# Kernel optimization log

Hardware: AMD Instinct MI355X
Metric: run time of the kernel (lower is better)

The kernel has to match this reference:

```python
import jax, jax.numpy as jnp
import numpy as np

EPS = 1e-5

def layer_norm(x, gamma, beta):
    mu = jnp.mean(x, axis=-1, keepdims=True)
    var = jnp.mean(jnp.square(x - mu), axis=-1, keepdims=True)
    return (x - mu) * jax.lax.rsqrt(var + EPS) * gamma + beta

def reverse_sigmoid(x):
    # torch version clamps value to [0.001, 0.999] with a detached offset ->
    # straight-through: clipped value, identity gradient into the logit.
    y = x + jax.lax.stop_gradient(jnp.clip(x, 0.001, 0.999) - x)
    return jnp.log(y) - jnp.log1p(-y)

def setup_inputs() -> dict:
    key = jax.random.key(0)
    ks = jax.random.split(key, 8)
    N, D, A, F8, FD = 32768, 1024, 256, 8, 64
    inp = {
        "unary_term": jax.random.normal(ks[0], (N, D), jnp.float32),
        "pair_term": jax.random.normal(ks[1], (N, D), jnp.float32),
        "auxiliary_term": jax.random.normal(ks[2], (N, A), jnp.float32),
        "auxiliary_gating_weight": jax.random.uniform(ks[3], (N,), jnp.float32),
        # self.w params: LayerNorm(2D) + Linear(2D, FD)
        "ln_gamma": jnp.ones((2 * D,), jnp.float32),
        "ln_beta": jnp.zeros((2 * D,), jnp.float32),
        "W": jax.random.normal(ks[4], (2 * D, FD), jnp.float32) * 0.02,
        "b": jnp.zeros((FD,), jnp.float32),
        # self.w_aux params: LayerNorm(A) + Linear(A, 8)
        "ln_aux_gamma": jnp.ones((A,), jnp.float32),
        "ln_aux_beta": jnp.zeros((A,), jnp.float32),
        "W_aux": jax.random.normal(ks[5], (A, F8), jnp.float32) * 0.02,
        "b_aux": jnp.zeros((F8,), jnp.float32),
        # use_auxiliary_gate_weight=True -> both init to 0.33
        "gate_weight": jnp.array(0.33, jnp.float32),
        "aux_gate_weight": jnp.array(0.33, jnp.float32),
    }
    return inp

def reference(unary_term, pair_term, auxiliary_term, auxiliary_gating_weight,
              ln_gamma, ln_beta, W, b, ln_aux_gamma, ln_aux_beta, W_aux, b_aux,
              gate_weight, aux_gate_weight):
    # paired_feats = relu(cat([unary, pair], 1))
    paired = jax.nn.relu(jnp.concatenate([unary_term, pair_term], axis=1))  # [N, 2D]
    # gate = sigmoid(Linear(relu(LN(paired))))
    gate = jax.nn.sigmoid(jax.nn.relu(layer_norm(paired, ln_gamma, ln_beta)) @ W + b)  # [N, FD]
    aux_gate = jax.nn.sigmoid(jax.nn.relu(layer_norm(auxiliary_term, ln_aux_gamma, ln_aux_beta)) @ W_aux + b_aux)  # [N, 8]
    gate = jnp.mean(gate, axis=1)        # [N]
    aux_gate = jnp.mean(aux_gate, axis=1)  # [N]
    logit = gate_weight * reverse_sigmoid(gate) + aux_gate_weight * reverse_sigmoid(aux_gate)
    g = jax.nn.sigmoid(logit) * auxiliary_gating_weight  # use_auxiliary_gate_weight=True
    output = pair_term * g[:, None]
    return (output, g)
```

## Files before the change

### kernel.cpp

```cpp
#include <hip/hip_runtime.h>
#include <math.h>


#define EPS_LN 1e-5f

typedef __attribute__((ext_vector_type(8))) short short8;
typedef __attribute__((ext_vector_type(4))) float f32x4;

__device__ __forceinline__ unsigned short f2bf(float f) {
  unsigned int u = __float_as_uint(f);
  u += 0x7FFFu + ((u >> 16) & 1u);
  return (unsigned short)(u >> 16);
}

__device__ __forceinline__ float wsum64(float v) {
  v += __shfl_xor(v, 32);
  v += __shfl_xor(v, 16);
  v += __shfl_xor(v, 8);
  v += __shfl_xor(v, 4);
  v += __shfl_xor(v, 2);
  v += __shfl_xor(v, 1);
  return v;
}

__device__ __forceinline__ float sigmoidf_(float x) {
  return 1.0f / (1.0f + __expf(-x));
}

__device__ __forceinline__ float rsigf(float x) {
  float y = fminf(fmaxf(x, 0.001f), 0.999f);
  return logf(y) - log1pf(-y);
}

__device__ __forceinline__ ushort4 norm_pack(float4 x, float4 g, float4 b,
                                             float mu, float rstd) {
  ushort4 o;
  o.x = f2bf(fmaxf((x.x - mu) * rstd * g.x + b.x, 0.f));
  o.y = f2bf(fmaxf((x.y - mu) * rstd * g.y + b.y, 0.f));
  o.z = f2bf(fmaxf((x.z - mu) * rstd * g.z + b.z, 0.f));
  o.w = f2bf(fmaxf((x.w - mu) * rstd * g.w + b.w, 0.f));
  return o;
}

__global__ void prep_wfrag(const float* __restrict__ W,
                           unsigned short* __restrict__ wfrag) {
  const int lane = threadIdx.x;
  const int b = blockIdx.x;
  const int ntile = b >> 6;
  const int kb = b & 63;
  const int f = (ntile << 4) + (lane & 15);
  const int kbase = (kb << 5) + ((lane >> 4) << 3);
  unsigned short tmp[8];
#pragma unroll
  for (int j = 0; j < 8; ++j) tmp[j] = f2bf(W[(size_t)(kbase + j) * 64 + f]);
  ushort4* dst = reinterpret_cast<ushort4*>(wfrag + (((size_t)b * 64 + lane) << 3));
  dst[0] = make_ushort4(tmp[0], tmp[1], tmp[2], tmp[3]);
  dst[1] = make_ushort4(tmp[4], tmp[5], tmp[6], tmp[7]);
}

__global__ void __launch_bounds__(256, 2) fused_main(
    const float* __restrict__ unary, const float* __restrict__ pair,
    const float* __restrict__ aux, const float* __restrict__ auxw,
    const float* __restrict__ ln_g, const float* __restrict__ ln_b,
    const float* __restrict__ b_lin,
    const float* __restrict__ ln_ag, const float* __restrict__ ln_ab,
    const float* __restrict__ W_aux, const float* __restrict__ b_aux,
    const float* __restrict__ gw, const float* __restrict__ agw,
    const unsigned short* __restrict__ wfrag,
    float* __restrict__ out, float* __restrict__ out_g) {
  __shared__ unsigned short act_lds[16 * 2048];

  const int tid = threadIdx.x;
  const int w = tid >> 6;
  const int lane = tid & 63;
  const int base = blockIdx.x << 4;

  float auxg0 = 0.f, auxg1 = 0.f, auxg2 = 0.f, auxg3 = 0.f;

#pragma unroll
  for (int i = 0; i < 4; ++i) {
    const int rl = (w << 2) + i;
    const int row = base + rl;
    const int sw = rl & 7;

    const float4* u4 = reinterpret_cast<const float4*>(unary + (size_t)row * 1024);
    const float4* p4 = reinterpret_cast<const float4*>(pair + (size_t)row * 1024);
    float4 uv[4], pv[4];
#pragma unroll
    for (int j = 0; j < 4; ++j) {
      uv[j] = u4[lane + 64 * j];
      pv[j] = p4[lane + 64 * j];
    }
    float s = 0.f, sq = 0.f;
#pragma unroll
    for (int j = 0; j < 4; ++j) {
      uv[j].x = fmaxf(uv[j].x, 0.f); uv[j].y = fmaxf(uv[j].y, 0.f);
      uv[j].z = fmaxf(uv[j].z, 0.f); uv[j].w = fmaxf(uv[j].w, 0.f);
      pv[j].x = fmaxf(pv[j].x, 0.f); pv[j].y = fmaxf(pv[j].y, 0.f);
      pv[j].z = fmaxf(pv[j].z, 0.f); pv[j].w = fmaxf(pv[j].w, 0.f);
      s += uv[j].x + uv[j].y + uv[j].z + uv[j].w;
      s += pv[j].x + pv[j].y + pv[j].z + pv[j].w;
      sq += uv[j].x * uv[j].x + uv[j].y * uv[j].y + uv[j].z * uv[j].z + uv[j].w * uv[j].w;
      sq += pv[j].x * pv[j].x + pv[j].y * pv[j].y + pv[j].z * pv[j].z + pv[j].w * pv[j].w;
    }
    s = wsum64(s);
    sq = wsum64(sq);
    const float mu = s * (1.f / 2048.f);
    const float rstd = rsqrtf(sq * (1.f / 2048.f) - mu * mu + EPS_LN);

    const float4* g4 = reinterpret_cast<const float4*>(ln_g);
    const float4* bb4 = reinterpret_cast<const float4*>(ln_b);
#pragma unroll
    for (int j = 0; j < 4; ++j) {
      const int idx = lane + 64 * j;
      const int off = (lane & 1) << 2;
      ushort4 o = norm_pack(uv[j], g4[idx], bb4[idx], mu, rstd);
      int addr = (rl << 11) + ((((idx >> 1)) ^ sw) << 3) + off;
      *reinterpret_cast<ushort4*>(&act_lds[addr]) = o;
      ushort4 o2 = norm_pack(pv[j], g4[256 + idx], bb4[256 + idx], mu, rstd);
      int addr2 = (rl << 11) + (((128 + (idx >> 1)) ^ sw) << 3) + off;
      *reinterpret_cast<ushort4*>(&act_lds[addr2]) = o2;
    }

    const float4 av = reinterpret_cast<const float4*>(aux + (size_t)row * 256)[lane];
    float as = av.x + av.y + av.z + av.w;
    float asq = av.x * av.x + av.y * av.y + av.z * av.z + av.w * av.w;
    as = wsum64(as);
    asq = wsum64(asq);
    const float amu = as * (1.f / 256.f);
    const float arstd = rsqrtf(asq * (1.f / 256.f) - amu * amu + EPS_LN);
    const float4 ag = reinterpret_cast<const float4*>(ln_ag)[lane];
    const float4 ab = reinterpret_cast<const float4*>(ln_ab)[lane];
    float aa[4];
    aa[0] = fmaxf((av.x - amu) * arstd * ag.x + ab.x, 0.f);
    aa[1] = fmaxf((av.y - amu) * arstd * ag.y + ab.y, 0.f);
    aa[2] = fmaxf((av.z - amu) * arstd * ag.z + ab.z, 0.f);
    aa[3] = fmaxf((av.w - amu) * arstd * ag.w + ab.w, 0.f);
    float pf[8];
#pragma unroll
    for (int f = 0; f < 8; ++f) pf[f] = 0.f;
#pragma unroll
    for (int t = 0; t < 4; ++t) {
      const float4* wr = reinterpret_cast<const float4*>(W_aux + (((size_t)lane << 2) + t) * 8);
      float4 wa = wr[0], wb = wr[1];
      pf[0] += aa[t] * wa.x; pf[1] += aa[t] * wa.y;
      pf[2] += aa[t] * wa.z; pf[3] += aa[t] * wa.w;
      pf[4] += aa[t] * wb.x; pf[5] += aa[t] * wb.y;
      pf[6] += aa[t] * wb.z; pf[7] += aa[t] * wb.w;
    }
    float ss = 0.f;
#pragma unroll
    for (int f = 0; f < 8; ++f) {
      float v = wsum64(pf[f]);
      ss += sigmoidf_(v + b_aux[f]);
    }
    const float agv = ss * (1.f / 8.f);
    if (i == 0) auxg0 = agv;
    else if (i == 1) auxg1 = agv;
    else if (i == 2) auxg2 = agv;
    else auxg3 = agv;
  }

  __syncthreads();

  f32x4 acc = {0.f, 0.f, 0.f, 0.f};
  const int arow = lane & 15;
  const int quad = lane >> 4;
  const int abase = arow << 11;
  const int asw = arow & 7;
  const unsigned short* wbase = wfrag + ((size_t)(w << 6) << 9);
#pragma unroll 8
  for (int kb = 0; kb < 64; ++kb) {
    const int c = (kb << 2) + quad;
    const short8 afrag =
        *reinterpret_cast<const short8*>(&act_lds[abase + ((c ^ asw) << 3)]);
    const short8 bfrag =
        *reinterpret_cast<const short8*>(wbase + ((size_t)kb << 9) + (lane << 3));
    acc = __builtin_amdgcn_mfma_f32_16x16x32_bf16(afrag, bfrag, acc, 0, 0, 0);
  }

  const float bl = b_lin[(w << 4) + arow];
  float sred[4];
#pragma unroll
  for (int i = 0; i < 4; ++i) {
    float v = sigmoidf_(acc[i] + bl);
    v += __shfl_xor(v, 1);
    v += __shfl_xor(v, 2);
    v += __shfl_xor(v, 4);
    v += __shfl_xor(v, 8);
    sred[i] = v;
  }

  __syncthreads();
  float* gate_part = reinterpret_cast<float*>(act_lds);
  if (arow == 0) {
#pragma unroll
    for (int i = 0; i < 4; ++i)
      gate_part[(w << 4) + (quad << 2) + i] = sred[i];
  }
  __syncthreads();

  const float gwt = gw[0];
  const float agwt = agw[0];
#pragma unroll
  for (int i = 0; i < 4; ++i) {
    const int rl = (w << 2) + i;
    const int row = base + rl;
    const float gsum = gate_part[rl] + gate_part[16 + rl] +
                       gate_part[32 + rl] + gate_part[48 + rl];
    const float gate = gsum * (1.f / 64.f);
    const float auxg = (i == 0) ? auxg0 : (i == 1) ? auxg1 : (i == 2) ? auxg2 : auxg3;
    const float logit = gwt * rsigf(gate) + agwt * rsigf(auxg);
    const float g = sigmoidf_(logit) * auxw[row];

    const float4* p4 = reinterpret_cast<const float4*>(pair + (size_t)row * 1024);
    float4* o4 = reinterpret_cast<float4*>(out + (size_t)row * 1024);
#pragma unroll
    for (int j = 0; j < 4; ++j) {
      float4 pv = p4[lane + 64 * j];
      pv.x *= g; pv.y *= g; pv.z *= g; pv.w *= g;
      o4[lane + 64 * j] = pv;
    }
    if (lane == 0) out_g[row] = g;
  }
}

extern "C" void kernel_launch(void* const* d_in, const int* in_sizes, int n_in,
                              void* d_out, int out_size, void* d_ws, size_t ws_size,
                              hipStream_t stream) {
  const float* unary = (const float*)d_in[0];
  const float* pair  = (const float*)d_in[1];
  const float* aux   = (const float*)d_in[2];
  const float* auxw  = (const float*)d_in[3];
  const float* ln_g  = (const float*)d_in[4];
  const float* ln_b  = (const float*)d_in[5];
  const float* W     = (const float*)d_in[6];
  const float* b     = (const float*)d_in[7];
  const float* ln_ag = (const float*)d_in[8];
  const float* ln_ab = (const float*)d_in[9];
  const float* W_aux = (const float*)d_in[10];
  const float* b_aux = (const float*)d_in[11];
  const float* gw    = (const float*)d_in[12];
  const float* agw   = (const float*)d_in[13];

  const int N = in_sizes[3];
  unsigned short* wfrag = (unsigned short*)d_ws;
  float* out = (float*)d_out;
  float* out_g = out + (size_t)N * 1024;

  prep_wfrag<<<256, 64, 0, stream>>>(W, wfrag);
  fused_main<<<N / 16, 256, 0, stream>>>(unary, pair, aux, auxw, ln_g, ln_b, b,
                                         ln_ag, ln_ab, W_aux, b_aux, gw, agw,
                                         wfrag, out, out_g);
}
```

Before: 480.0 us.

## Drop activation LDS staging; recompute normalized inputs straight into MFMA fragments

The 64KB bf16 activation buffer in shared memory is replaced by small per-row stats and a partial-sum array. In the GEMM phase each wave re-reads its quarter of the K dimension from global memory (expected L2 hits), normalizes it in registers, and feeds four N-tiles of MFMA, with cross-wave K partials reduced through LDS. The smaller LDS footprint allows the launch bound to rise to 4 blocks per CU. The aux-gate reduction is also restructured to use fewer shuffles. The cost is a second read of unary/pair rows and extra normalization arithmetic.

Result: faster. 435.8 us (-9.2%).

```diff
diff --git a/kernel.cpp b/kernel.cpp
--- a/kernel.cpp
+++ b/kernel.cpp
@@ -32,14 +32,12 @@
   return logf(y) - log1pf(-y);
 }
 
-__device__ __forceinline__ ushort4 norm_pack(float4 x, float4 g, float4 b,
-                                             float mu, float rstd) {
-  ushort4 o;
-  o.x = f2bf(fmaxf((x.x - mu) * rstd * g.x + b.x, 0.f));
-  o.y = f2bf(fmaxf((x.y - mu) * rstd * g.y + b.y, 0.f));
-  o.z = f2bf(fmaxf((x.z - mu) * rstd * g.z + b.z, 0.f));
-  o.w = f2bf(fmaxf((x.w - mu) * rstd * g.w + b.w, 0.f));
-  return o;
+__device__ __forceinline__ short nrm1(float x, float g, float b,
+                                      float rs, float nmr) {
+  float t = fmaxf(x, 0.f);
+  float n = fmaf(t, rs, nmr);
+  float z = fmaxf(fmaf(n, g, b), 0.f);
+  return (short)f2bf(z);
 }
 
 __global__ void prep_wfrag(const float* __restrict__ W,
@@ -58,7 +56,7 @@
   dst[1] = make_ushort4(tmp[4], tmp[5], tmp[6], tmp[7]);
 }
 
-__global__ void __launch_bounds__(256, 2) fused_main(
+__global__ void __launch_bounds__(256, 4) fused_main(
     const float* __restrict__ unary, const float* __restrict__ pair,
     const float* __restrict__ aux, const float* __restrict__ auxw,
     const float* __restrict__ ln_g, const float* __restrict__ ln_b,
@@ -68,7 +66,9 @@
     const float* __restrict__ gw, const float* __restrict__ agw,
     const unsigned short* __restrict__ wfrag,
     float* __restrict__ out, float* __restrict__ out_g) {
-  __shared__ unsigned short act_lds[16 * 2048];
+  __shared__ float part[4][16][68];
+  __shared__ float stat_mu[16];
+  __shared__ float stat_rs[16];
 
   const int tid = threadIdx.x;
   const int w = tid >> 6;
@@ -77,50 +77,36 @@
 
   float auxg0 = 0.f, auxg1 = 0.f, auxg2 = 0.f, auxg3 = 0.f;
 
+  const float4 agv4 = reinterpret_cast<const float4*>(ln_ag)[lane];
+  const float4 abv4 = reinterpret_cast<const float4*>(ln_ab)[lane];
+  const float bauxl = b_aux[lane & 7];
+
 #pragma unroll
   for (int i = 0; i < 4; ++i) {
     const int rl = (w << 2) + i;
     const int row = base + rl;
-    const int sw = rl & 7;
 
     const float4* u4 = reinterpret_cast<const float4*>(unary + (size_t)row * 1024);
     const float4* p4 = reinterpret_cast<const float4*>(pair + (size_t)row * 1024);
-    float4 uv[4], pv[4];
+    float s = 0.f, sq = 0.f;
 #pragma unroll
     for (int j = 0; j < 4; ++j) {
-      uv[j] = u4[lane + 64 * j];
-      pv[j] = p4[lane + 64 * j];
-    }
-    float s = 0.f, sq = 0.f;
-#pragma unroll
-    for (int j = 0; j < 4; ++j) {
-      uv[j].x = fmaxf(uv[j].x, 0.f); uv[j].y = fmaxf(uv[j].y, 0.f);
-      uv[j].z = fmaxf(uv[j].z, 0.f); uv[j].w = fmaxf(uv[j].w, 0.f);
-      pv[j].x = fmaxf(pv[j].x, 0.f); pv[j].y = fmaxf(pv[j].y, 0.f);
-      pv[j].z = fmaxf(pv[j].z, 0.f); pv[j].w = fmaxf(pv[j].w, 0.f);
-      s += uv[j].x + uv[j].y + uv[j].z + uv[j].w;
-      s += pv[j].x + pv[j].y + pv[j].z + pv[j].w;
-      sq += uv[j].x * uv[j].x + uv[j].y * uv[j].y + uv[j].z * uv[j].z + uv[j].w * uv[j].w;
-      sq += pv[j].x * pv[j].x + pv[j].y * pv[j].y + pv[j].z * pv[j].z + pv[j].w * pv[j].w;
+      float4 uv = u4[lane + 64 * j];
+      float4 pv = p4[lane + 64 * j];
+      uv.x = fmaxf(uv.x, 0.f); uv.y = fmaxf(uv.y, 0.f);
+      uv.z = fmaxf(uv.z, 0.f); uv.w = fmaxf(uv.w, 0.f);
+      pv.x = fmaxf(pv.x, 0.f); pv.y = fmaxf(pv.y, 0.f);
+      pv.z = fmaxf(pv.z, 0.f); pv.w = fmaxf(pv.w, 0.f);
+      s += uv.x + uv.y + uv.z + uv.w;
+      s += pv.x + pv.y + pv.z + pv.w;
+      sq += uv.x * uv.x + uv.y * uv.y + uv.z * uv.z + uv.w * uv.w;
+      sq += pv.x * pv.x + pv.y * pv.y + pv.z * pv.z + pv.w * pv.w;
     }
     s = wsum64(s);
     sq = wsum64(sq);
     const float mu = s * (1.f / 2048.f);
     const float rstd = rsqrtf(sq * (1.f / 2048.f) - mu * mu + EPS_LN);
-
-    const float4* g4 = reinterpret_cast<const float4*>(ln_g);
-    const float4* bb4 = reinterpret_cast<const float4*>(ln_b);
-#pragma unroll
-    for (int j = 0; j < 4; ++j) {
-      const int idx = lane + 64 * j;
-      const int off = (lane & 1) << 2;
-      ushort4 o = norm_pack(uv[j], g4[idx], bb4[idx], mu, rstd);
-      int addr = (rl << 11) + ((((idx >> 1)) ^ sw) << 3) + off;
-      *reinterpret_cast<ushort4*>(&act_lds[addr]) = o;
-      ushort4 o2 = norm_pack(pv[j], g4[256 + idx], bb4[256 + idx], mu, rstd);
-      int addr2 = (rl << 11) + (((128 + (idx >> 1)) ^ sw) << 3) + off;
-      *reinterpret_cast<ushort4*>(&act_lds[addr2]) = o2;
-    }
+    if (lane == 0) { stat_mu[rl] = mu; stat_rs[rl] = rstd; }
 
     const float4 av = reinterpret_cast<const float4*>(aux + (size_t)row * 256)[lane];
     float as = av.x + av.y + av.z + av.w;
@@ -129,13 +115,11 @@
     asq = wsum64(asq);
     const float amu = as * (1.f / 256.f);
     const float arstd = rsqrtf(asq * (1.f / 256.f) - amu * amu + EPS_LN);
-    const float4 ag = reinterpret_cast<const float4*>(ln_ag)[lane];
-    const float4 ab = reinterpret_cast<const float4*>(ln_ab)[lane];
     float aa[4];
-    aa[0] = fmaxf((av.x - amu) * arstd * ag.x + ab.x, 0.f);
-    aa[1] = fmaxf((av.y - amu) * arstd * ag.y + ab.y, 0.f);
-    aa[2] = fmaxf((av.z - amu) * arstd * ag.z + ab.z, 0.f);
-    aa[3] = fmaxf((av.w - amu) * arstd * ag.w + ab.w, 0.f);
+    aa[0] = fmaxf((av.x - amu) * arstd * agv4.x + abv4.x, 0.f);
+    aa[1] = fmaxf((av.y - amu) * arstd * agv4.y + abv4.y, 0.f);
+    aa[2] = fmaxf((av.z - amu) * arstd * agv4.z + abv4.z, 0.f);
+    aa[3] = fmaxf((av.w - amu) * arstd * agv4.w + abv4.w, 0.f);
     float pf[8];
 #pragma unroll
     for (int f = 0; f < 8; ++f) pf[f] = 0.f;
@@ -148,13 +132,27 @@
       pf[4] += aa[t] * wb.x; pf[5] += aa[t] * wb.y;
       pf[6] += aa[t] * wb.z; pf[7] += aa[t] * wb.w;
     }
-    float ss = 0.f;
 #pragma unroll
     for (int f = 0; f < 8; ++f) {
-      float v = wsum64(pf[f]);
-      ss += sigmoidf_(v + b_aux[f]);
-    }
-    const float agv = ss * (1.f / 8.f);
+      pf[f] += __shfl_xor(pf[f], 1);
+      pf[f] += __shfl_xor(pf[f], 2);
+      pf[f] += __shfl_xor(pf[f], 4);
+    }
+    float v01 = (lane & 1) ? pf[1] : pf[0];
+    float v23 = (lane & 1) ? pf[3] : pf[2];
+    float v45 = (lane & 1) ? pf[5] : pf[4];
+    float v67 = (lane & 1) ? pf[7] : pf[6];
+    float v03 = (lane & 2) ? v23 : v01;
+    float v47 = (lane & 2) ? v67 : v45;
+    float v = (lane & 4) ? v47 : v03;
+    v += __shfl_xor(v, 8);
+    v += __shfl_xor(v, 16);
+    v += __shfl_xor(v, 32);
+    float sg = sigmoidf_(v + bauxl);
+    sg += __shfl_xor(sg, 1);
+    sg += __shfl_xor(sg, 2);
+    sg += __shfl_xor(sg, 4);
+    const float agv = sg * 0.125f;
     if (i == 0) auxg0 = agv;
     else if (i == 1) auxg1 = agv;
     else if (i == 2) auxg2 = agv;
@@ -163,65 +161,87 @@
 
   __syncthreads();
 
-  f32x4 acc = {0.f, 0.f, 0.f, 0.f};
-  const int arow = lane & 15;
-  const int quad = lane >> 4;
-  const int abase = arow << 11;
-  const int asw = arow & 7;
-  const unsigned short* wbase = wfrag + ((size_t)(w << 6) << 9);
-#pragma unroll 8
-  for (int kb = 0; kb < 64; ++kb) {
-    const int c = (kb << 2) + quad;
-    const short8 afrag =
-        *reinterpret_cast<const short8*>(&act_lds[abase + ((c ^ asw) << 3)]);
-    const short8 bfrag =
-        *reinterpret_cast<const short8*>(wbase + ((size_t)kb << 9) + (lane << 3));
-    acc = __builtin_amdgcn_mfma_f32_16x16x32_bf16(afrag, bfrag, acc, 0, 0, 0);
+  const int m = lane & 15;
+  const int q = lane >> 4;
+  const float mu = stat_mu[m];
+  const float rs = stat_rs[m];
+  const float nmr = -mu * rs;
+
+  const float* srcp = (w < 2) ? unary : pair;
+  const float* rowp = srcp + (size_t)(base + m) * 1024 + ((w & 1) << 9) + (q << 3);
+  const float* gp = ln_g + (w << 9) + (q << 3);
+  const float* bp = ln_b + (w << 9) + (q << 3);
+  const unsigned short* wfp = wfrag + ((size_t)((w << 4) * 64 + lane) << 3);
+
+  f32x4 acc[4] = {{0.f,0.f,0.f,0.f},{0.f,0.f,0.f,0.f},
+                  {0.f,0.f,0.f,0.f},{0.f,0.f,0.f,0.f}};
+#pragma unroll
+  for (int kb = 0; kb < 16; ++kb) {
+    const float4 x0 = *reinterpret_cast<const float4*>(rowp + (kb << 5));
+    const float4 x1 = *reinterpret_cast<const float4*>(rowp + (kb << 5) + 4);
+    const float4 g0 = *reinterpret_cast<const float4*>(gp + (kb << 5));
+    const float4 g1 = *reinterpret_cast<const float4*>(gp + (kb << 5) + 4);
+    const float4 b0 = *reinterpret_cast<const float4*>(bp + (kb << 5));
+    const float4 b1 = *reinterpret_cast<const float4*>(bp + (kb << 5) + 4);
+    short8 af;
+    af[0] = nrm1(x0.x, g0.x, b0.x, rs, nmr);
+    af[1] = nrm1(x0.y, g0.y, b0.y, rs, nmr);
+    af[2] = nrm1(x0.z, g0.z, b0.z, rs, nmr);
+    af[3] = nrm1(x0.w, g0.w, b0.w, rs, nmr);
+    af[4] = nrm1(x1.x, g1.x, b1.x, rs, nmr);
+    af[5] = nrm1(x1.y, g1.y, b1.y, rs, nmr);
+    af[6] = nrm1(x1.z, g1.z, b1.z, rs, nmr);
+    af[7] = nrm1(x1.w, g1.w, b1.w, rs, nmr);
+#pragma unroll
+    for (int nt = 0; nt < 4; ++nt) {
+      const short8 bf = *reinterpret_cast<const short8*>(
+          wfp + (size_t)nt * 32768 + (kb << 9));
+      acc[nt] = __builtin_amdgcn_mfma_f32_16x16x32_bf16(af, bf, acc[nt], 0, 0, 0);
+    }
   }
 
-  const float bl = b_lin[(w << 4) + arow];
-  float sred[4];
+#pragma unroll
+  for (int nt = 0; nt < 4; ++nt)
+#pragma unroll
+    for (int r = 0; r < 4; ++r)
+      part[w][(q << 2) + r][(nt << 4) + m] = acc[nt][r];
+
+  __syncthreads();
+
+  const int rl = (w << 2) + q;
+  const int f0 = m << 2;
+  const float4 p0 = *reinterpret_cast<const float4*>(&part[0][rl][f0]);
+  const float4 p1 = *reinterpret_cast<const float4*>(&part[1][rl][f0]);
+  const float4 p2 = *reinterpret_cast<const float4*>(&part[2][rl][f0]);
+  const float4 p3 = *reinterpret_cast<const float4*>(&part[3][rl][f0]);
+  const float4 blv = reinterpret_cast<const float4*>(b_lin)[m];
+  float sgs = sigmoidf_(p0.x + p1.x + p2.x + p3.x + blv.x)
+            + sigmoidf_(p0.y + p1.y + p2.y + p3.y + blv.y)
+            + sigmoidf_(p0.z + p1.z + p2.z + p3.z + blv.z)
+            + sigmoidf_(p0.w + p1.w + p2.w + p3.w + blv.w);
+  sgs += __shfl_xor(sgs, 1);
+  sgs += __shfl_xor(sgs, 2);
+  sgs += __shfl_xor(sgs, 4);
+  sgs += __shfl_xor(sgs, 8);
+  const float gate = sgs * (1.f / 64.f);
+  const float auxg_r = (q == 0) ? auxg0 : (q == 1) ? auxg1
+                     : (q == 2) ? auxg2 : auxg3;
+  const float logit = gw[0] * rsigf(gate) + agw[0] * rsigf(auxg_r);
+  const float g = sigmoidf_(logit) * auxw[base + rl];
+  if (m == 0) out_g[base + rl] = g;
+
 #pragma unroll
   for (int i = 0; i < 4; ++i) {
-    float v = sigmoidf_(acc[i] + bl);
-    v += __shfl_xor(v, 1);
-    v += __shfl_xor(v, 2);
-    v += __shfl_xor(v, 4);
-    v += __shfl_xor(v, 8);
-    sred[i] = v;
-  }
-
-  __syncthreads();
-  float* gate_part = reinterpret_cast<float*>(act_lds);
-  if (arow == 0) {
-#pragma unroll
-    for (int i = 0; i < 4; ++i)
-      gate_part[(w << 4) + (quad << 2) + i] = sred[i];
-  }
-  __syncthreads();
-
-  const float gwt = gw[0];
-  const float agwt = agw[0];
-#pragma unroll
-  for (int i = 0; i < 4; ++i) {
-    const int rl = (w << 2) + i;
-    const int row = base + rl;
-    const float gsum = gate_part[rl] + gate_part[16 + rl] +
-                       gate_part[32 + rl] + gate_part[48 + rl];
-    const float gate = gsum * (1.f / 64.f);
-    const float auxg = (i == 0) ? auxg0 : (i == 1) ? auxg1 : (i == 2) ? auxg2 : auxg3;
-    const float logit = gwt * rsigf(gate) + agwt * rsigf(auxg);
-    const float g = sigmoidf_(logit) * auxw[row];
-
-    const float4* p4 = reinterpret_cast<const float4*>(pair + (size_t)row * 1024);
-    float4* o4 = reinterpret_cast<float4*>(out + (size_t)row * 1024);
+    const float gi = __shfl(g, i << 4);
+    const int row = base + (w << 2) + i;
+    const float4* pp = reinterpret_cast<const float4*>(pair + (size_t)row * 1024);
+    float4* oo = reinterpret_cast<float4*>(out + (size_t)row * 1024);
 #pragma unroll
     for (int j = 0; j < 4; ++j) {
-      float4 pv = p4[lane + 64 * j];
-      pv.x *= g; pv.y *= g; pv.z *= g; pv.w *= g;
-      o4[lane + 64 * j] = pv;
-    }
-    if (lane == 0) out_g[row] = g;
+      float4 pv = pp[lane + (j << 6)];
+      pv.x *= gi; pv.y *= gi; pv.z *= gi; pv.w *= gi;
+      oo[lane + (j << 6)] = pv;
+    }
   }
 }
 
```
